# Kernel tuning notes

Hardware: AMD Instinct MI355X
Metric: run time of the kernel (lower is better)

The kernel has to match this reference:

```python
import jax, jax.numpy as jnp
import numpy as np

SINKHORN_ALPHA = 20.0
WEIGHT_LOSS_ECR = 100.0
OT_MAX_ITER = 100
STOP_THR = 0.005
EPS = 1e-16


def setup_inputs() -> dict:
    key = jax.random.key(0)
    # cost matrix: [num_topics, vocab]
    M = jax.random.uniform(key, (512, 65536), dtype=jnp.float32)
    return {"M": M}


def reference(M) -> jnp.ndarray:
    n, m = M.shape
    a = jnp.full((n, 1), 1.0 / n, dtype=M.dtype)   # row marginal
    b = jnp.full((m, 1), 1.0 / m, dtype=M.dtype)   # col marginal
    u0 = jnp.full((n, 1), 1.0 / n, dtype=M.dtype)
    K = jnp.exp(-M * SINKHORN_ALPHA)               # [n, m]

    def cond_fn(carry):
        u, v, err, cpt = carry
        return (err > STOP_THR) & (cpt < OT_MAX_ITER)

    def body_fn(carry):
        u, v, err, cpt = carry
        v = b / (K.T @ u + EPS)                    # [m, 1]
        u = a / (K @ v + EPS)                      # [n, 1]
        cpt = cpt + 1
        # convergence check every 50 iters (cpt % 50 == 1), matching torch loop
        err = jax.lax.cond(
            cpt % 50 == 1,
            lambda: jnp.sum(jnp.abs(v * (K.T @ u) - b)).astype(err.dtype),
            lambda: err,
        )
        return (u, v, err, cpt)

    init = (u0, jnp.zeros((m, 1), dtype=M.dtype), jnp.asarray(1.0, M.dtype), jnp.asarray(0, jnp.int32))
    u, v, _, _ = jax.lax.while_loop(cond_fn, body_fn, init)

    transp = u * (K * v.T)                         # [n, m] transport plan
    loss_ECR = jnp.sum(transp * M) * WEIGHT_LOSS_ECR
    return loss_ECR
```

## Files before the change

### kernel.cpp

```cpp
#include <hip/hip_runtime.h>
#include <hip/hip_cooperative_groups.h>

namespace cg = cooperative_groups;

#define NROW 512
#define NCOL 65536

static __device__ __forceinline__ float wave_sum(float x) {
  #pragma unroll
  for (int off = 32; off; off >>= 1) x += __shfl_down(x, off, 64);
  return x;
}

__global__ __launch_bounds__(256)
void k1_colsum(const float* __restrict__ M, float* __restrict__ v,
               float* __restrict__ eA) {
  const int tid = threadIdx.x, bid = blockIdx.x;
  const int chunk = tid & 15;
  const int part  = tid >> 4;
  const int col0  = (bid << 6) + (chunk << 2);
  const int r0    = part << 5;
  const float am = 1.0f / NROW, bm = 1.0f / NCOL, EPSV = 1e-16f;

  __shared__ float sCol[16 * 64];

  if (bid == 0 && tid < 3) eA[tid] = 0.f;

  float4 cs = {0.f, 0.f, 0.f, 0.f};
  #pragma unroll 8
  for (int r = r0; r < r0 + 32; ++r) {
    float4 m = *(const float4*)(M + (size_t)r * NCOL + col0);
    cs.x += __expf(-20.f * m.x);
    cs.y += __expf(-20.f * m.y);
    cs.z += __expf(-20.f * m.z);
    cs.w += __expf(-20.f * m.w);
  }
  *(float4*)(sCol + part * 64 + (chunk << 2)) = cs;
  __syncthreads();
  if (tid < 64) {
    float t = 0.f;
    #pragma unroll
    for (int p = 0; p < 16; ++p) t += sCol[p * 64 + tid];
    v[(bid << 6) + tid] = bm / (t * am + EPSV);
  }
}

__global__ __launch_bounds__(256)
void k2_rowdot(const float* __restrict__ M, const float* __restrict__ v,
               float* __restrict__ u) {
  const int tid = threadIdx.x, row = blockIdx.x;
  const float am = 1.0f / NROW, EPSV = 1e-16f;
  const float4* M4 = (const float4*)M + (size_t)row * (NCOL / 4);
  const float4* V4 = (const float4*)v;
  __shared__ float sRed[4];

  float acc = 0.f;
  #pragma unroll 8
  for (int it = 0; it < NCOL / 4 / 256; ++it) {
    const int c = (it << 8) + tid;
    float4 m = M4[c];
    float4 vv = V4[c];
    acc += __expf(-20.f * m.x) * vv.x + __expf(-20.f * m.y) * vv.y
         + __expf(-20.f * m.z) * vv.z + __expf(-20.f * m.w) * vv.w;
  }
  acc = wave_sum(acc);
  if ((tid & 63) == 0) sRed[tid >> 6] = acc;
  __syncthreads();
  if (tid == 0)
    u[row] = am / (sRed[0] + sRed[1] + sRed[2] + sRed[3] + EPSV);
}

__global__ __launch_bounds__(256)
void k3_fused(const float* __restrict__ M, const float* __restrict__ v,
              const float* __restrict__ u, float* __restrict__ tArr,
              float* __restrict__ eA) {
  const int tid = threadIdx.x, bid = blockIdx.x;
  const int chunk = tid & 15;
  const int part  = tid >> 4;
  const int col0  = (bid << 6) + (chunk << 2);
  const int r0    = part << 5;
  const float bm = 1.0f / NCOL;

  __shared__ float sU[NROW];
  __shared__ float sCol[16 * 64];
  __shared__ float sRed[4];

  sU[tid] = u[tid];
  sU[tid + 256] = u[tid + 256];
  __syncthreads();

  const float4 vv = *(const float4*)(v + col0);
  float4 cs = {0.f, 0.f, 0.f, 0.f};
  float lacc = 0.f;
  #pragma unroll 8
  for (int r = r0; r < r0 + 32; ++r) {
    float4 m = *(const float4*)(M + (size_t)r * NCOL + col0);
    float e0 = __expf(-20.f * m.x), e1 = __expf(-20.f * m.y);
    float e2 = __expf(-20.f * m.z), e3 = __expf(-20.f * m.w);
    float us = sU[r];
    cs.x = fmaf(e0, us, cs.x);
    cs.y = fmaf(e1, us, cs.y);
    cs.z = fmaf(e2, us, cs.z);
    cs.w = fmaf(e3, us, cs.w);
    lacc += us * (e0 * m.x * vv.x + e1 * m.y * vv.y
                + e2 * m.z * vv.z + e3 * m.w * vv.w);
  }
  *(float4*)(sCol + part * 64 + (chunk << 2)) = cs;
  lacc = wave_sum(lacc);
  if ((tid & 63) == 0) sRed[tid >> 6] = lacc;
  __syncthreads();

  float pe = 0.f;
  if (tid < 64) {
    float t = 0.f;
    #pragma unroll
    for (int p = 0; p < 16; ++p) t += sCol[p * 64 + tid];
    tArr[(bid << 6) + tid] = t;
    pe = fabsf(v[(bid << 6) + tid] * t - bm);
    pe = wave_sum(pe);
  }
  if (tid == 0) {
    atomicAdd(&eA[0], pe);
    atomicAdd(&eA[2], sRed[0] + sRed[1] + sRed[2] + sRed[3]);
  }
}

__global__ void k4_decide(const float* __restrict__ eA, float* __restrict__ out,
                          int* __restrict__ done) {
  if (threadIdx.x == 0) {
    if (eA[0] <= 0.005f) { out[0] = 100.f * eA[2]; done[0] = 1; }
    else                 { out[0] = 0.f;           done[0] = 0; }
  }
}

__global__ __launch_bounds__(1024)
void k5_fallback(const float* __restrict__ M, float* __restrict__ out,
                 float* __restrict__ v, float* __restrict__ u,
                 const float* __restrict__ tArr, float* __restrict__ eA,
                 const int* __restrict__ done) {
  if (done[0]) return;
  cg::grid_group grid = cg::this_grid();
  const int tid = threadIdx.x, bid = blockIdx.x;
  const float am = 1.0f / NROW, bm = 1.0f / NCOL, EPSV = 1e-16f;

  __shared__ float sU[NROW];
  __shared__ float sCol[16 * 256];
  __shared__ float sRedA[16], sRedB[16];

  const int chunk = tid & 63;
  const int part  = tid >> 6;
  const int col0  = (bid << 8) + (chunk << 2);
  const int r0    = part << 5;
  const int row0  = bid << 1;

  float tt = (tid < 256) ? tArr[(bid << 8) + tid] : 0.f;

  int cpt = 1;
  while (true) {
    if (tid < 256) v[(bid << 8) + tid] = bm / (tt + EPSV);
    grid.sync();
    cpt++;

    {
      const float4* M40 = (const float4*)M + (size_t)row0 * (NCOL / 4);
      const float4* M41 = (const float4*)M + (size_t)(row0 + 1) * (NCOL / 4);
      const float4* V4  = (const float4*)v;
      float ra = 0.f, rb = 0.f;
      #pragma unroll 4
      for (int it = 0; it < NCOL / 4 / 1024; ++it) {
        const int c = (it << 10) + tid;
        float4 vv = V4[c];
        float4 m0 = M40[c], m1 = M41[c];
        ra += __expf(-20.f * m0.x) * vv.x + __expf(-20.f * m0.y) * vv.y
            + __expf(-20.f * m0.z) * vv.z + __expf(-20.f * m0.w) * vv.w;
        rb += __expf(-20.f * m1.x) * vv.x + __expf(-20.f * m1.y) * vv.y
            + __expf(-20.f * m1.z) * vv.z + __expf(-20.f * m1.w) * vv.w;
      }
      ra = wave_sum(ra); rb = wave_sum(rb);
      if ((tid & 63) == 0) { sRedA[tid >> 6] = ra; sRedB[tid >> 6] = rb; }
      __syncthreads();
      if (tid < 2) {
        const float* sr = (tid == 0) ? sRedA : sRedB;
        float s = 0.f;
        #pragma unroll
        for (int w = 0; w < 16; ++w) s += sr[w];
        u[row0 + tid] = am / (s + EPSV);
      }
    }
    grid.sync();
    if (cpt >= 100) break;

    if (tid < NROW) sU[tid] = u[tid];
    __syncthreads();
    float4 cs = {0.f, 0.f, 0.f, 0.f};
    #pragma unroll 4
    for (int r = r0; r < r0 + 32; ++r) {
      float4 m = *(const float4*)(M + (size_t)r * NCOL + col0);
      float us = sU[r];
      cs.x = fmaf(__expf(-20.f * m.x), us, cs.x);
      cs.y = fmaf(__expf(-20.f * m.y), us, cs.y);
      cs.z = fmaf(__expf(-20.f * m.z), us, cs.z);
      cs.w = fmaf(__expf(-20.f * m.w), us, cs.w);
    }
    *(float4*)(sCol + part * 256 + (chunk << 2)) = cs;
    __syncthreads();
    if (tid < 256) {
      tt = 0.f;
      #pragma unroll
      for (int p = 0; p < 16; ++p) tt += sCol[p * 256 + tid];
    }

    if (cpt == 51) {
      float pe = (tid < 256) ? fabsf(v[(bid << 8) + tid] * tt - bm) : 0.f;
      pe = wave_sum(pe);
      __syncthreads();
      if ((tid & 63) == 0) sRedA[tid >> 6] = pe;
      __syncthreads();
      if (tid == 0) {
        float s = 0.f;
        #pragma unroll
        for (int w = 0; w < 16; ++w) s += sRedA[w];
        atomicAdd(&eA[1], s);
      }
      grid.sync();
      if (eA[1] <= 0.005f) break;
    }
  }

  __syncthreads();
  if (tid < NROW) sU[tid] = u[tid];
  __syncthreads();
  {
    const float4 vv = *(const float4*)(v + col0);
    float lacc = 0.f;
    #pragma unroll 4
    for (int r = r0; r < r0 + 32; ++r) {
      float4 m = *(const float4*)(M + (size_t)r * NCOL + col0);
      float us = sU[r];
      lacc += us * (__expf(-20.f * m.x) * m.x * vv.x
                  + __expf(-20.f * m.y) * m.y * vv.y
                  + __expf(-20.f * m.z) * m.z * vv.z
                  + __expf(-20.f * m.w) * m.w * vv.w);
    }
    lacc = wave_sum(lacc);
    if ((tid & 63) == 0) sRedA[tid >> 6] = lacc;
    __syncthreads();
    if (tid == 0) {
      float s = 0.f;
      #pragma unroll
      for (int w = 0; w < 16; ++w) s += sRedA[w];
      atomicAdd(out, 100.f * s);
    }
  }
}

extern "C" void kernel_launch(void* const* d_in, const int* in_sizes, int n_in,
                              void* d_out, int out_size, void* d_ws, size_t ws_size,
                              hipStream_t stream) {
  const float* M = (const float*)d_in[0];
  float* out = (float*)d_out;

  const size_t offV = 0;
  const size_t offT = offV + (size_t)NCOL * sizeof(float);
  const size_t offU = offT + (size_t)NCOL * sizeof(float);
  const size_t offE = offU + 4096;
  const size_t offD = offE + 256;
  const size_t need = offD + 256;
  if (ws_size < need) return;

  char* ws = (char*)d_ws;
  float* v    = (float*)(ws + offV);
  float* tArr = (float*)(ws + offT);
  float* u    = (float*)(ws + offU);
  float* eA   = (float*)(ws + offE);
  int*   done = (int*)(ws + offD);

  k1_colsum<<<dim3(1024), dim3(256), 0, stream>>>(M, v, eA);
  k2_rowdot<<<dim3(512),  dim3(256), 0, stream>>>(M, v, u);
  k3_fused <<<dim3(1024), dim3(256), 0, stream>>>(M, v, u, tArr, eA);
  k4_decide<<<dim3(1),    dim3(64),  0, stream>>>(eA, out, done);

  void* args[] = { (void*)&M, (void*)&out, (void*)&v, (void*)&u,
                   (void*)&tArr, (void*)&eA, (void*)&done };
  hipLaunchCooperativeKernel((void*)k5_fallback, dim3(256), dim3(1024),
                             args, 0, stream);
}
```

Measured before the change: 274.6 us.

## Split column-sum passes into row bands with partial-sum reduction kernels

The column-reduction kernels (initial colsum and the fused K^T u / loss pass) now tile M into 8 row bands by 512-column blocks instead of full-height 64-column strips. Each block writes per-band partial column sums to a workspace buffer, and two small new kernels reduce the bands to produce v and the error term. The aim is wider, more contiguous row accesses (2KB per row segment instead of 256B) for better DRAM efficiency. The cost is two extra launches and extra partial-sum traffic, plus a larger workspace requirement.

```diff
diff --git a/kernel.cpp b/kernel.cpp
--- a/kernel.cpp
+++ b/kernel.cpp
@@ -5,6 +5,8 @@
 
 #define NROW 512
 #define NCOL 65536
+#define BANDS 8
+#define BPB   128
 
 static __device__ __forceinline__ float wave_sum(float x) {
   #pragma unroll
@@ -13,16 +15,16 @@
 }
 
 __global__ __launch_bounds__(256)
-void k1_colsum(const float* __restrict__ M, float* __restrict__ v,
-               float* __restrict__ eA) {
+void k1a_partial(const float* __restrict__ M, float* __restrict__ tPart,
+                 float* __restrict__ eA) {
   const int tid = threadIdx.x, bid = blockIdx.x;
-  const int chunk = tid & 15;
-  const int part  = tid >> 4;
-  const int col0  = (bid << 6) + (chunk << 2);
-  const int r0    = part << 5;
-  const float am = 1.0f / NROW, bm = 1.0f / NCOL, EPSV = 1e-16f;
-
-  __shared__ float sCol[16 * 64];
+  const int band = bid >> 7, blk = bid & 127;
+  const int chunk = tid & 127;
+  const int part  = tid >> 7;
+  const int col0  = (blk << 9) + (chunk << 2);
+  const int r0    = (band << 6) + (part << 5);
+
+  __shared__ float sCol[2 * 512];
 
   if (bid == 0 && tid < 3) eA[tid] = 0.f;
 
@@ -35,14 +37,30 @@
     cs.z += __expf(-20.f * m.z);
     cs.w += __expf(-20.f * m.w);
   }
-  *(float4*)(sCol + part * 64 + (chunk << 2)) = cs;
-  __syncthreads();
-  if (tid < 64) {
-    float t = 0.f;
-    #pragma unroll
-    for (int p = 0; p < 16; ++p) t += sCol[p * 64 + tid];
-    v[(bid << 6) + tid] = bm / (t * am + EPSV);
-  }
+  *(float4*)(sCol + part * 512 + (chunk << 2)) = cs;
+  __syncthreads();
+  if (tid < 128) {
+    float4 a = *(const float4*)(sCol + (tid << 2));
+    float4 b = *(const float4*)(sCol + 512 + (tid << 2));
+    float4 t = {a.x + b.x, a.y + b.y, a.z + b.z, a.w + b.w};
+    *(float4*)(tPart + (size_t)band * NCOL + (blk << 9) + (tid << 2)) = t;
+  }
+}
+
+__global__ __launch_bounds__(256)
+void k1b_v1(const float* __restrict__ tPart, float* __restrict__ v) {
+  const int gid = blockIdx.x * 256 + threadIdx.x;
+  const int col0 = gid << 2;
+  const float am = 1.0f / NROW, bm = 1.0f / NCOL, EPSV = 1e-16f;
+  float4 t = {0.f, 0.f, 0.f, 0.f};
+  #pragma unroll
+  for (int b = 0; b < BANDS; ++b) {
+    float4 p = *(const float4*)(tPart + (size_t)b * NCOL + col0);
+    t.x += p.x; t.y += p.y; t.z += p.z; t.w += p.w;
+  }
+  float4 vv = {bm / (t.x * am + EPSV), bm / (t.y * am + EPSV),
+               bm / (t.z * am + EPSV), bm / (t.w * am + EPSV)};
+  *(float4*)(v + col0) = vv;
 }
 
 __global__ __launch_bounds__(256)
@@ -71,33 +89,33 @@
 }
 
 __global__ __launch_bounds__(256)
-void k3_fused(const float* __restrict__ M, const float* __restrict__ v,
-              const float* __restrict__ u, float* __restrict__ tArr,
-              float* __restrict__ eA) {
+void k3a_partial(const float* __restrict__ M, const float* __restrict__ v,
+                 const float* __restrict__ u, float* __restrict__ tPart,
+                 float* __restrict__ eA) {
   const int tid = threadIdx.x, bid = blockIdx.x;
-  const int chunk = tid & 15;
-  const int part  = tid >> 4;
-  const int col0  = (bid << 6) + (chunk << 2);
-  const int r0    = part << 5;
-  const float bm = 1.0f / NCOL;
-
-  __shared__ float sU[NROW];
-  __shared__ float sCol[16 * 64];
+  const int band = bid >> 7, blk = bid & 127;
+  const int chunk = tid & 127;
+  const int part  = tid >> 7;
+  const int col0  = (blk << 9) + (chunk << 2);
+  const int r0l   = part << 5;
+
+  __shared__ float sU[64];
+  __shared__ float sCol[2 * 512];
   __shared__ float sRed[4];
 
-  sU[tid] = u[tid];
-  sU[tid + 256] = u[tid + 256];
+  if (tid < 64) sU[tid] = u[(band << 6) + tid];
   __syncthreads();
 
   const float4 vv = *(const float4*)(v + col0);
+  const float* Mb = M + (size_t)(band << 6) * NCOL;
   float4 cs = {0.f, 0.f, 0.f, 0.f};
   float lacc = 0.f;
   #pragma unroll 8
-  for (int r = r0; r < r0 + 32; ++r) {
-    float4 m = *(const float4*)(M + (size_t)r * NCOL + col0);
+  for (int rl = r0l; rl < r0l + 32; ++rl) {
+    float4 m = *(const float4*)(Mb + (size_t)rl * NCOL + col0);
     float e0 = __expf(-20.f * m.x), e1 = __expf(-20.f * m.y);
     float e2 = __expf(-20.f * m.z), e3 = __expf(-20.f * m.w);
-    float us = sU[r];
+    float us = sU[rl];
     cs.x = fmaf(e0, us, cs.x);
     cs.y = fmaf(e1, us, cs.y);
     cs.z = fmaf(e2, us, cs.z);
@@ -105,24 +123,44 @@
     lacc += us * (e0 * m.x * vv.x + e1 * m.y * vv.y
                 + e2 * m.z * vv.z + e3 * m.w * vv.w);
   }
-  *(float4*)(sCol + part * 64 + (chunk << 2)) = cs;
+  *(float4*)(sCol + part * 512 + (chunk << 2)) = cs;
   lacc = wave_sum(lacc);
   if ((tid & 63) == 0) sRed[tid >> 6] = lacc;
   __syncthreads();
-
-  float pe = 0.f;
-  if (tid < 64) {
-    float t = 0.f;
-    #pragma unroll
-    for (int p = 0; p < 16; ++p) t += sCol[p * 64 + tid];
-    tArr[(bid << 6) + tid] = t;
-    pe = fabsf(v[(bid << 6) + tid] * t - bm);
-    pe = wave_sum(pe);
-  }
-  if (tid == 0) {
-    atomicAdd(&eA[0], pe);
+  if (tid < 128) {
+    float4 a = *(const float4*)(sCol + (tid << 2));
+    float4 b = *(const float4*)(sCol + 512 + (tid << 2));
+    float4 t = {a.x + b.x, a.y + b.y, a.z + b.z, a.w + b.w};
+    *(float4*)(tPart + (size_t)band * NCOL + (blk << 9) + (tid << 2)) = t;
+  }
+  if (tid == 0)
     atomicAdd(&eA[2], sRed[0] + sRed[1] + sRed[2] + sRed[3]);
-  }
+}
+
+__global__ __launch_bounds__(256)
+void k3b_err(const float* __restrict__ tPart, const float* __restrict__ v,
+             float* __restrict__ tArr, float* __restrict__ eA) {
+  const int tid = threadIdx.x;
+  const int gid = blockIdx.x * 256 + tid;
+  const int col0 = gid << 2;
+  const float bm = 1.0f / NCOL;
+  __shared__ float sRed[4];
+
+  float4 t = {0.f, 0.f, 0.f, 0.f};
+  #pragma unroll
+  for (int b = 0; b < BANDS; ++b) {
+    float4 p = *(const float4*)(tPart + (size_t)b * NCOL + col0);
+    t.x += p.x; t.y += p.y; t.z += p.z; t.w += p.w;
+  }
+  *(float4*)(tArr + col0) = t;
+  float4 vv = *(const float4*)(v + col0);
+  float pe = fabsf(vv.x * t.x - bm) + fabsf(vv.y * t.y - bm)
+           + fabsf(vv.z * t.z - bm) + fabsf(vv.w * t.w - bm);
+  pe = wave_sum(pe);
+  if ((tid & 63) == 0) sRed[tid >> 6] = pe;
+  __syncthreads();
+  if (tid == 0)
+    atomicAdd(&eA[0], sRed[0] + sRed[1] + sRed[2] + sRed[3]);
 }
 
 __global__ void k4_decide(const float* __restrict__ eA, float* __restrict__ out,
@@ -265,20 +303,24 @@
   const size_t offU = offT + (size_t)NCOL * sizeof(float);
   const size_t offE = offU + 4096;
   const size_t offD = offE + 256;
-  const size_t need = offD + 256;
+  const size_t offP = offD + 256;
+  const size_t need = offP + (size_t)BANDS * NCOL * sizeof(float);
   if (ws_size < need) return;
 
   char* ws = (char*)d_ws;
-  float* v    = (float*)(ws + offV);
-  float* tArr = (float*)(ws + offT);
-  float* u    = (float*)(ws + offU);
-  float* eA   = (float*)(ws + offE);
-  int*   done = (int*)(ws + offD);
-
-  k1_colsum<<<dim3(1024), dim3(256), 0, stream>>>(M, v, eA);
-  k2_rowdot<<<dim3(512),  dim3(256), 0, stream>>>(M, v, u);
-  k3_fused <<<dim3(1024), dim3(256), 0, stream>>>(M, v, u, tArr, eA);
-  k4_decide<<<dim3(1),    dim3(64),  0, stream>>>(eA, out, done);
+  float* v     = (float*)(ws + offV);
+  float* tArr  = (float*)(ws + offT);
+  float* u     = (float*)(ws + offU);
+  float* eA    = (float*)(ws + offE);
+  int*   done  = (int*)(ws + offD);
+  float* tPart = (float*)(ws + offP);
+
+  k1a_partial<<<dim3(1024), dim3(256), 0, stream>>>(M, tPart, eA);
+  k1b_v1     <<<dim3(64),   dim3(256), 0, stream>>>(tPart, v);
+  k2_rowdot  <<<dim3(512),  dim3(256), 0, stream>>>(M, v, u);
+  k3a_partial<<<dim3(1024), dim3(256), 0, stream>>>(M, v, u, tPart, eA);
+  k3b_err    <<<dim3(64),   dim3(256), 0, stream>>>(tPart, v, tArr, eA);
+  k4_decide  <<<dim3(1),    dim3(64),  0, stream>>>(eA, out, done);
 
   void* args[] = { (void*)&M, (void*)&out, (void*)&v, (void*)&u,
                    (void*)&tArr, (void*)&eA, (void*)&done };
```

Result: no change. 272.8 us (-0.7%).

## Materialize exp(-20M) once in fp16 and recover loss via log identity

Applied to the files above, without the earlier changes.

Builds an fp16 copy of K=exp(-20M) in the first pass, together with column sums via atomics. Later passes stream the half-size K instead of rereading fp32 M and recomputing exp. The loss term M*K is rewritten as -K*log(K)/20, so the final reduction needs only K, and the M*K*v reduction is folded into the row-dot pass as a per-row partial weighted later by u. This lowers memory traffic and exp work, at the cost of fp16 rounding of K (values below the fp16 range flush to zero or lose precision), extra 64MB workspace, and atomics plus a memset.

```diff
diff --git a/kernel.cpp b/kernel.cpp
--- a/kernel.cpp
+++ b/kernel.cpp
@@ -1,4 +1,5 @@
 #include <hip/hip_runtime.h>
+#include <hip/hip_fp16.h>
 #include <hip/hip_cooperative_groups.h>
 
 namespace cg = cooperative_groups;
@@ -12,131 +13,187 @@
   return x;
 }
 
-__global__ __launch_bounds__(256)
-void k1_colsum(const float* __restrict__ M, float* __restrict__ v,
-               float* __restrict__ eA) {
+static __device__ __forceinline__ float dot8h(uint4 e, const float4& va, const float4& vb) {
+  const __half2* hp = (const __half2*)&e;
+  float2 f0 = __half22float2(hp[0]), f1 = __half22float2(hp[1]);
+  float2 f2 = __half22float2(hp[2]), f3 = __half22float2(hp[3]);
+  return f0.x*va.x + f0.y*va.y + f1.x*va.z + f1.y*va.w
+       + f2.x*vb.x + f2.y*vb.y + f3.x*vb.z + f3.y*vb.w;
+}
+
+__global__ __launch_bounds__(256)
+void n1_build(const float* __restrict__ M, __half* __restrict__ Eh,
+              float* __restrict__ t0) {
   const int tid = threadIdx.x, bid = blockIdx.x;
-  const int chunk = tid & 15;
-  const int part  = tid >> 4;
-  const int col0  = (bid << 6) + (chunk << 2);
-  const int r0    = part << 5;
-  const float am = 1.0f / NROW, bm = 1.0f / NCOL, EPSV = 1e-16f;
-
-  __shared__ float sCol[16 * 64];
-
-  if (bid == 0 && tid < 3) eA[tid] = 0.f;
+  const int band = bid >> 7, blk = bid & 127;
+  const int chunk = tid & 127, part = tid >> 7;
+  const int col0 = (blk << 9) + (chunk << 2);
+  const int r0   = (band << 6) + (part << 5);
+
+  __shared__ float sCol[2 * 512];
 
   float4 cs = {0.f, 0.f, 0.f, 0.f};
   #pragma unroll 8
   for (int r = r0; r < r0 + 32; ++r) {
     float4 m = *(const float4*)(M + (size_t)r * NCOL + col0);
-    cs.x += __expf(-20.f * m.x);
-    cs.y += __expf(-20.f * m.y);
-    cs.z += __expf(-20.f * m.z);
-    cs.w += __expf(-20.f * m.w);
-  }
-  *(float4*)(sCol + part * 64 + (chunk << 2)) = cs;
-  __syncthreads();
+    __half2 hv[2];
+    hv[0] = __floats2half2_rn(__expf(-20.f * m.x), __expf(-20.f * m.y));
+    hv[1] = __floats2half2_rn(__expf(-20.f * m.z), __expf(-20.f * m.w));
+    *(float2*)(Eh + (size_t)r * NCOL + col0) = *(float2*)hv;
+    float2 f0 = __half22float2(hv[0]), f1 = __half22float2(hv[1]);
+    cs.x += f0.x; cs.y += f0.y; cs.z += f1.x; cs.w += f1.y;
+  }
+  *(float4*)(sCol + part * 512 + (chunk << 2)) = cs;
+  __syncthreads();
+  if (tid < 128) {
+    float4 a = *(const float4*)(sCol + (tid << 2));
+    float4 b = *(const float4*)(sCol + 512 + (tid << 2));
+    float* dst = t0 + (blk << 9) + (tid << 2);
+    atomicAdd(dst + 0, a.x + b.x);
+    atomicAdd(dst + 1, a.y + b.y);
+    atomicAdd(dst + 2, a.z + b.z);
+    atomicAdd(dst + 3, a.w + b.w);
+  }
+}
+
+__global__ __launch_bounds__(256)
+void n2_rowdot(const __half* __restrict__ Eh, const float* __restrict__ t0,
+               float* __restrict__ sPart, float* __restrict__ wPart) {
+  const int tid = threadIdx.x, bid = blockIdx.x;
+  const int row = bid >> 1, half_ = bid & 1;
+  const int cbase = half_ * (NCOL / 2);
+  const float am = 1.0f / NROW, bm = 1.0f / NCOL, EPSV = 1e-16f;
+
+  const uint4*  E4 = (const uint4*)(Eh + (size_t)row * NCOL + cbase);
+  const float4* T4 = (const float4*)(t0 + cbase);
+  __shared__ float sRed[8];
+
+  float s = 0.f, w = 0.f;
+  #pragma unroll 4
+  for (int it = 0; it < 16; ++it) {
+    const int c = (it << 8) + tid;
+    uint4 er = E4[c];
+    float4 ta = T4[2*c], tb = T4[2*c + 1];
+    float4 va = {bm / (ta.x*am + EPSV), bm / (ta.y*am + EPSV),
+                 bm / (ta.z*am + EPSV), bm / (ta.w*am + EPSV)};
+    float4 vb = {bm / (tb.x*am + EPSV), bm / (tb.y*am + EPSV),
+                 bm / (tb.z*am + EPSV), bm / (tb.w*am + EPSV)};
+    const __half2* hp = (const __half2*)&er;
+    float2 f0 = __half22float2(hp[0]), f1 = __half22float2(hp[1]);
+    float2 f2 = __half22float2(hp[2]), f3 = __half22float2(hp[3]);
+    s += f0.x*va.x + f0.y*va.y + f1.x*va.z + f1.y*va.w
+       + f2.x*vb.x + f2.y*vb.y + f3.x*vb.z + f3.y*vb.w;
+    w += f0.x*va.x*__logf(fmaxf(f0.x, 1e-12f))
+       + f0.y*va.y*__logf(fmaxf(f0.y, 1e-12f))
+       + f1.x*va.z*__logf(fmaxf(f1.x, 1e-12f))
+       + f1.y*va.w*__logf(fmaxf(f1.y, 1e-12f))
+       + f2.x*vb.x*__logf(fmaxf(f2.x, 1e-12f))
+       + f2.y*vb.y*__logf(fmaxf(f2.y, 1e-12f))
+       + f3.x*vb.z*__logf(fmaxf(f3.x, 1e-12f))
+       + f3.y*vb.w*__logf(fmaxf(f3.y, 1e-12f));
+  }
+  s = wave_sum(s); w = wave_sum(w);
+  if ((tid & 63) == 0) { sRed[tid >> 6] = s; sRed[4 + (tid >> 6)] = w; }
+  __syncthreads();
+  if (tid == 0) sPart[bid] = sRed[0] + sRed[1] + sRed[2] + sRed[3];
+  if (tid == 1) wPart[bid] = sRed[4] + sRed[5] + sRed[6] + sRed[7];
+}
+
+__global__ __launch_bounds__(256)
+void n3_colsum2(const __half* __restrict__ Eh, const float* __restrict__ sPart,
+                float* __restrict__ u, float* __restrict__ t2) {
+  const int tid = threadIdx.x, bid = blockIdx.x;
+  const int band = bid >> 7, blk = bid & 127;
+  const int chunk = tid & 63, part = tid >> 6;
+  const int col0 = (blk << 9) + (chunk << 3);
+  const float am = 1.0f / NROW, EPSV = 1e-16f;
+
+  __shared__ float sU[64];
+  __shared__ float sCol[4 * 512];
+
   if (tid < 64) {
-    float t = 0.f;
-    #pragma unroll
-    for (int p = 0; p < 16; ++p) t += sCol[p * 64 + tid];
-    v[(bid << 6) + tid] = bm / (t * am + EPSV);
-  }
-}
-
-__global__ __launch_bounds__(256)
-void k2_rowdot(const float* __restrict__ M, const float* __restrict__ v,
-               float* __restrict__ u) {
-  const int tid = threadIdx.x, row = blockIdx.x;
-  const float am = 1.0f / NROW, EPSV = 1e-16f;
-  const float4* M4 = (const float4*)M + (size_t)row * (NCOL / 4);
-  const float4* V4 = (const float4*)v;
+    const int i = (band << 6) + tid;
+    float s = sPart[2*i] + sPart[2*i + 1];
+    float uv = am / (s + EPSV);
+    sU[tid] = uv;
+    if (blk == 0) u[i] = uv;
+  }
+  __syncthreads();
+
+  float c0=0,c1=0,c2=0,c3=0,c4=0,c5=0,c6=0,c7=0;
+  const __half* Eb = Eh + (size_t)(band << 6) * NCOL + col0;
+  #pragma unroll 8
+  for (int rl = part * 16; rl < part * 16 + 16; ++rl) {
+    uint4 er = *(const uint4*)(Eb + (size_t)rl * NCOL);
+    const __half2* hp = (const __half2*)&er;
+    float2 f0 = __half22float2(hp[0]), f1 = __half22float2(hp[1]);
+    float2 f2 = __half22float2(hp[2]), f3 = __half22float2(hp[3]);
+    float us = sU[rl];
+    c0 = fmaf(f0.x, us, c0); c1 = fmaf(f0.y, us, c1);
+    c2 = fmaf(f1.x, us, c2); c3 = fmaf(f1.y, us, c3);
+    c4 = fmaf(f2.x, us, c4); c5 = fmaf(f2.y, us, c5);
+    c6 = fmaf(f3.x, us, c6); c7 = fmaf(f3.y, us, c7);
+  }
+  float* sc = sCol + part * 512 + (chunk << 3);
+  sc[0]=c0; sc[1]=c1; sc[2]=c2; sc[3]=c3; sc[4]=c4; sc[5]=c5; sc[6]=c6; sc[7]=c7;
+  __syncthreads();
+  if (tid < 128) {
+    const int lc = tid << 2;
+    float4 a = *(const float4*)(sCol + lc);
+    float4 b = *(const float4*)(sCol + 512 + lc);
+    float4 c = *(const float4*)(sCol + 1024 + lc);
+    float4 d = *(const float4*)(sCol + 1536 + lc);
+    float* dst = t2 + (blk << 9) + lc;
+    atomicAdd(dst + 0, a.x + b.x + c.x + d.x);
+    atomicAdd(dst + 1, a.y + b.y + c.y + d.y);
+    atomicAdd(dst + 2, a.z + b.z + c.z + d.z);
+    atomicAdd(dst + 3, a.w + b.w + c.w + d.w);
+  }
+}
+
+__global__ __launch_bounds__(256)
+void n4_err(const float* __restrict__ t0, const float* __restrict__ t2,
+            float* __restrict__ v, float* __restrict__ eA) {
+  const int tid = threadIdx.x;
+  const int col0 = (blockIdx.x * 256 + tid) << 2;
+  const float am = 1.0f / NROW, bm = 1.0f / NCOL, EPSV = 1e-16f;
   __shared__ float sRed[4];
 
-  float acc = 0.f;
-  #pragma unroll 8
-  for (int it = 0; it < NCOL / 4 / 256; ++it) {
-    const int c = (it << 8) + tid;
-    float4 m = M4[c];
-    float4 vv = V4[c];
-    acc += __expf(-20.f * m.x) * vv.x + __expf(-20.f * m.y) * vv.y
-         + __expf(-20.f * m.z) * vv.z + __expf(-20.f * m.w) * vv.w;
-  }
-  acc = wave_sum(acc);
-  if ((tid & 63) == 0) sRed[tid >> 6] = acc;
-  __syncthreads();
-  if (tid == 0)
-    u[row] = am / (sRed[0] + sRed[1] + sRed[2] + sRed[3] + EPSV);
-}
-
-__global__ __launch_bounds__(256)
-void k3_fused(const float* __restrict__ M, const float* __restrict__ v,
-              const float* __restrict__ u, float* __restrict__ tArr,
-              float* __restrict__ eA) {
-  const int tid = threadIdx.x, bid = blockIdx.x;
-  const int chunk = tid & 15;
-  const int part  = tid >> 4;
-  const int col0  = (bid << 6) + (chunk << 2);
-  const int r0    = part << 5;
-  const float bm = 1.0f / NCOL;
-
-  __shared__ float sU[NROW];
-  __shared__ float sCol[16 * 64];
+  float4 t = *(const float4*)(t0 + col0);
+  float4 s = *(const float4*)(t2 + col0);
+  float4 vv = {bm / (t.x*am + EPSV), bm / (t.y*am + EPSV),
+               bm / (t.z*am + EPSV), bm / (t.w*am + EPSV)};
+  *(float4*)(v + col0) = vv;
+  float pe = fabsf(vv.x*s.x - bm) + fabsf(vv.y*s.y - bm)
+           + fabsf(vv.z*s.z - bm) + fabsf(vv.w*s.w - bm);
+  pe = wave_sum(pe);
+  if ((tid & 63) == 0) sRed[tid >> 6] = pe;
+  __syncthreads();
+  if (tid == 0) atomicAdd(&eA[0], sRed[0] + sRed[1] + sRed[2] + sRed[3]);
+}
+
+__global__ __launch_bounds__(256)
+void n5_decide(const float* __restrict__ eA, const float* __restrict__ u,
+               const float* __restrict__ wPart, float* __restrict__ out,
+               int* __restrict__ done) {
+  const int tid = threadIdx.x;
   __shared__ float sRed[4];
-
-  sU[tid] = u[tid];
-  sU[tid + 256] = u[tid + 256];
-  __syncthreads();
-
-  const float4 vv = *(const float4*)(v + col0);
-  float4 cs = {0.f, 0.f, 0.f, 0.f};
-  float lacc = 0.f;
-  #pragma unroll 8
-  for (int r = r0; r < r0 + 32; ++r) {
-    float4 m = *(const float4*)(M + (size_t)r * NCOL + col0);
-    float e0 = __expf(-20.f * m.x), e1 = __expf(-20.f * m.y);
-    float e2 = __expf(-20.f * m.z), e3 = __expf(-20.f * m.w);
-    float us = sU[r];
-    cs.x = fmaf(e0, us, cs.x);
-    cs.y = fmaf(e1, us, cs.y);
-    cs.z = fmaf(e2, us, cs.z);
-    cs.w = fmaf(e3, us, cs.w);
-    lacc += us * (e0 * m.x * vv.x + e1 * m.y * vv.y
-                + e2 * m.z * vv.z + e3 * m.w * vv.w);
-  }
-  *(float4*)(sCol + part * 64 + (chunk << 2)) = cs;
-  lacc = wave_sum(lacc);
-  if ((tid & 63) == 0) sRed[tid >> 6] = lacc;
-  __syncthreads();
-
-  float pe = 0.f;
-  if (tid < 64) {
-    float t = 0.f;
-    #pragma unroll
-    for (int p = 0; p < 16; ++p) t += sCol[p * 64 + tid];
-    tArr[(bid << 6) + tid] = t;
-    pe = fabsf(v[(bid << 6) + tid] * t - bm);
-    pe = wave_sum(pe);
-  }
+  float l = u[2*tid]     * (wPart[4*tid]     + wPart[4*tid + 1])
+          + u[2*tid + 1] * (wPart[4*tid + 2] + wPart[4*tid + 3]);
+  l = wave_sum(l);
+  if ((tid & 63) == 0) sRed[tid >> 6] = l;
+  __syncthreads();
   if (tid == 0) {
-    atomicAdd(&eA[0], pe);
-    atomicAdd(&eA[2], sRed[0] + sRed[1] + sRed[2] + sRed[3]);
-  }
-}
-
-__global__ void k4_decide(const float* __restrict__ eA, float* __restrict__ out,
-                          int* __restrict__ done) {
-  if (threadIdx.x == 0) {
-    if (eA[0] <= 0.005f) { out[0] = 100.f * eA[2]; done[0] = 1; }
-    else                 { out[0] = 0.f;           done[0] = 0; }
+    float loss = -5.0f * (sRed[0] + sRed[1] + sRed[2] + sRed[3]);
+    if (eA[0] <= 0.005f) { out[0] = loss; done[0] = 1; }
+    else                 { out[0] = 0.f;  done[0] = 0; }
   }
 }
 
 __global__ __launch_bounds__(1024)
-void k5_fallback(const float* __restrict__ M, float* __restrict__ out,
+void n6_fallback(const __half* __restrict__ Eh, float* __restrict__ out,
                  float* __restrict__ v, float* __restrict__ u,
-                 const float* __restrict__ tArr, float* __restrict__ eA,
+                 const float* __restrict__ t2, float* __restrict__ eA,
                  const int* __restrict__ done) {
   if (done[0]) return;
   cg::grid_group grid = cg::this_grid();
@@ -144,16 +201,14 @@
   const float am = 1.0f / NROW, bm = 1.0f / NCOL, EPSV = 1e-16f;
 
   __shared__ float sU[NROW];
-  __shared__ float sCol[16 * 256];
+  __shared__ float sCol[32 * 256];
   __shared__ float sRedA[16], sRedB[16];
 
-  const int chunk = tid & 63;
-  const int part  = tid >> 6;
-  const int col0  = (bid << 8) + (chunk << 2);
-  const int r0    = part << 5;
-  const int row0  = bid << 1;
-
-  float tt = (tid < 256) ? tArr[(bid << 8) + tid] : 0.f;
+  const int chunk = tid & 31, part = tid >> 5;
+  const int col0 = (bid << 8) + (chunk << 3);
+  const int row0 = bid << 1;
+
+  float tt = (tid < 256) ? t2[(bid << 8) + tid] : 0.f;
 
   int cpt = 1;
   while (true) {
@@ -162,19 +217,16 @@
     cpt++;
 
     {
-      const float4* M40 = (const float4*)M + (size_t)row0 * (NCOL / 4);
-      const float4* M41 = (const float4*)M + (size_t)(row0 + 1) * (NCOL / 4);
+      const uint4*  E40 = (const uint4*)(Eh + (size_t)row0 * NCOL);
+      const uint4*  E41 = (const uint4*)(Eh + (size_t)(row0 + 1) * NCOL);
       const float4* V4  = (const float4*)v;
       float ra = 0.f, rb = 0.f;
       #pragma unroll 4
-      for (int it = 0; it < NCOL / 4 / 1024; ++it) {
+      for (int it = 0; it < NCOL / 8 / 1024; ++it) {
         const int c = (it << 10) + tid;
-        float4 vv = V4[c];
-        float4 m0 = M40[c], m1 = M41[c];
-        ra += __expf(-20.f * m0.x) * vv.x + __expf(-20.f * m0.y) * vv.y
-            + __expf(-20.f * m0.z) * vv.z + __expf(-20.f * m0.w) * vv.w;
-        rb += __expf(-20.f * m1.x) * vv.x + __expf(-20.f * m1.y) * vv.y
-            + __expf(-20.f * m1.z) * vv.z + __expf(-20.f * m1.w) * vv.w;
+        float4 va = V4[2*c], vb = V4[2*c + 1];
+        ra += dot8h(E40[c], va, vb);
+        rb += dot8h(E41[c], va, vb);
       }
       ra = wave_sum(ra); rb = wave_sum(rb);
       if ((tid & 63) == 0) { sRedA[tid >> 6] = ra; sRedB[tid >> 6] = rb; }
@@ -192,22 +244,31 @@
 
     if (tid < NROW) sU[tid] = u[tid];
     __syncthreads();
-    float4 cs = {0.f, 0.f, 0.f, 0.f};
+    float cs[8];
+    #pragma unroll
+    for (int k = 0; k < 8; ++k) cs[k] = 0.f;
     #pragma unroll 4
-    for (int r = r0; r < r0 + 32; ++r) {
-      float4 m = *(const float4*)(M + (size_t)r * NCOL + col0);
-      float us = sU[r];
-      cs.x = fmaf(__expf(-20.f * m.x), us, cs.x);
-      cs.y = fmaf(__expf(-20.f * m.y), us, cs.y);
-      cs.z = fmaf(__expf(-20.f * m.z), us, cs.z);
-      cs.w = fmaf(__expf(-20.f * m.w), us, cs.w);
-    }
-    *(float4*)(sCol + part * 256 + (chunk << 2)) = cs;
+    for (int rl = part * 16; rl < part * 16 + 16; ++rl) {
+      uint4 er = *(const uint4*)(Eh + (size_t)rl * NCOL + col0);
+      const __half2* hp = (const __half2*)&er;
+      float2 f0 = __half22float2(hp[0]), f1 = __half22float2(hp[1]);
+      float2 f2 = __half22float2(hp[2]), f3 = __half22float2(hp[3]);
+      float us = sU[rl];
+      cs[0] = fmaf(f0.x, us, cs[0]); cs[1] = fmaf(f0.y, us, cs[1]);
+      cs[2] = fmaf(f1.x, us, cs[2]); cs[3] = fmaf(f1.y, us, cs[3]);
+      cs[4] = fmaf(f2.x, us, cs[4]); cs[5] = fmaf(f2.y, us, cs[5]);
+      cs[6] = fmaf(f3.x, us, cs[6]); cs[7] = fmaf(f3.y, us, cs[7]);
+    }
+    {
+      float* sc = sCol + part * 256 + (chunk << 3);
+      #pragma unroll
+      for (int k = 0; k < 8; ++k) sc[k] = cs[k];
+    }
     __syncthreads();
     if (tid < 256) {
       tt = 0.f;
       #pragma unroll
-      for (int p = 0; p < 16; ++p) tt += sCol[p * 256 + tid];
+      for (int p = 0; p < 32; ++p) tt += sCol[p * 256 + tid];
     }
 
     if (cpt == 51) {
@@ -231,16 +292,24 @@
   if (tid < NROW) sU[tid] = u[tid];
   __syncthreads();
   {
-    const float4 vv = *(const float4*)(v + col0);
+    float4 va = *(const float4*)(v + col0);
+    float4 vb = *(const float4*)(v + col0 + 4);
     float lacc = 0.f;
     #pragma unroll 4
-    for (int r = r0; r < r0 + 32; ++r) {
-      float4 m = *(const float4*)(M + (size_t)r * NCOL + col0);
-      float us = sU[r];
-      lacc += us * (__expf(-20.f * m.x) * m.x * vv.x
-                  + __expf(-20.f * m.y) * m.y * vv.y
-                  + __expf(-20.f * m.z) * m.z * vv.z
-                  + __expf(-20.f * m.w) * m.w * vv.w);
+    for (int rl = part * 16; rl < part * 16 + 16; ++rl) {
+      uint4 er = *(const uint4*)(Eh + (size_t)rl * NCOL + col0);
+      const __half2* hp = (const __half2*)&er;
+      float2 f0 = __half22float2(hp[0]), f1 = __half22float2(hp[1]);
+      float2 f2 = __half22float2(hp[2]), f3 = __half22float2(hp[3]);
+      float us = sU[rl];
+      lacc += us * (f0.x*va.x*__logf(fmaxf(f0.x, 1e-12f))
+                  + f0.y*va.y*__logf(fmaxf(f0.y, 1e-12f))
+                  + f1.x*va.z*__logf(fmaxf(f1.x, 1e-12f))
+                  + f1.y*va.w*__logf(fmaxf(f1.y, 1e-12f))
+                  + f2.x*vb.x*__logf(fmaxf(f2.x, 1e-12f))
+                  + f2.y*vb.y*__logf(fmaxf(f2.y, 1e-12f))
+                  + f3.x*vb.z*__logf(fmaxf(f3.x, 1e-12f))
+                  + f3.y*vb.w*__logf(fmaxf(f3.y, 1e-12f)));
     }
     lacc = wave_sum(lacc);
     if ((tid & 63) == 0) sRedA[tid >> 6] = lacc;
@@ -249,7 +318,7 @@
       float s = 0.f;
       #pragma unroll
       for (int w = 0; w < 16; ++w) s += sRedA[w];
-      atomicAdd(out, 100.f * s);
+      atomicAdd(out, -5.0f * s);
     }
   }
 }
@@ -260,28 +329,39 @@
   const float* M = (const float*)d_in[0];
   float* out = (float*)d_out;
 
-  const size_t offV = 0;
-  const size_t offT = offV + (size_t)NCOL * sizeof(float);
-  const size_t offU = offT + (size_t)NCOL * sizeof(float);
-  const size_t offE = offU + 4096;
-  const size_t offD = offE + 256;
-  const size_t need = offD + 256;
+  const size_t offEh = 0;
+  const size_t offT0 = offEh + (size_t)NROW * NCOL * sizeof(__half);
+  const size_t offT2 = offT0 + (size_t)NCOL * sizeof(float);
+  const size_t offEA = offT2 + (size_t)NCOL * sizeof(float);
+  const size_t offDN = offEA + 256;
+  const size_t offSP = offDN + 256;
+  const size_t offWP = offSP + 4096;
+  const size_t offU  = offWP + 4096;
+  const size_t offV  = offU  + 2048;
+  const size_t need  = offV + (size_t)NCOL * sizeof(float);
   if (ws_size < need) return;
 
   char* ws = (char*)d_ws;
-  float* v    = (float*)(ws + offV);
-  float* tArr = (float*)(ws + offT);
-  float* u    = (float*)(ws + offU);
-  float* eA   = (float*)(ws + offE);
-  int*   done = (int*)(ws + offD);
-
-  k1_colsum<<<dim3(1024), dim3(256), 0, stream>>>(M, v, eA);
-  k2_rowdot<<<dim3(512),  dim3(256), 0, stream>>>(M, v, u);
-  k3_fused <<<dim3(1024), dim3(256), 0, stream>>>(M, v, u, tArr, eA);
-  k4_decide<<<dim3(1),    dim3(64),  0, stream>>>(eA, out, done);
-
-  void* args[] = { (void*)&M, (void*)&out, (void*)&v, (void*)&u,
-                   (void*)&tArr, (void*)&eA, (void*)&done };
-  hipLaunchCooperativeKernel((void*)k5_fallback, dim3(256), dim3(1024),
+  __half* Eh   = (__half*)(ws + offEh);
+  float* t0    = (float*)(ws + offT0);
+  float* t2    = (float*)(ws + offT2);
+  float* eA    = (float*)(ws + offEA);
+  int*   done  = (int*)(ws + offDN);
+  float* sPart = (float*)(ws + offSP);
+  float* wPart = (float*)(ws + offWP);
+  float* u     = (float*)(ws + offU);
+  float* v     = (float*)(ws + offV);
+
+  hipMemsetAsync(ws + offT0, 0, 2 * (size_t)NCOL * sizeof(float) + 256, stream);
+
+  n1_build  <<<dim3(1024), dim3(256), 0, stream>>>(M, Eh, t0);
+  n2_rowdot <<<dim3(1024), dim3(256), 0, stream>>>(Eh, t0, sPart, wPart);
+  n3_colsum2<<<dim3(1024), dim3(256), 0, stream>>>(Eh, sPart, u, t2);
+  n4_err    <<<dim3(64),   dim3(256), 0, stream>>>(t0, t2, v, eA);
+  n5_decide <<<dim3(1),    dim3(256), 0, stream>>>(eA, u, wPart, out, done);
+
+  void* args[] = { (void*)&Eh, (void*)&out, (void*)&v, (void*)&u,
+                   (void*)&t2, (void*)&eA, (void*)&done };
+  hipLaunchCooperativeKernel((void*)n6_fallback, dim3(256), dim3(1024),
                              args, 0, stream);
 }
```

Result: slower. 287.2 us (+4.6%).
